# Kernel optimization log

Measured on AMD Instinct MI355X. Metric: run time of the kernel, lower is better.

## Reference

```python
import jax, jax.numpy as jnp
import numpy as np

S = 14          # grid size
B = 2           # boxes per cell
NCLS = 20       # number of classes
L_COORD = 5.0
L_NOOBJ = 0.5


def setup_inputs() -> dict:
    key = jax.random.key(0)
    k1, k2, k3, k4 = jax.random.split(key, 4)
    N = 4096
    pred_tensor = jax.random.uniform(k1, (N, S, S, B * 5 + NCLS), dtype=jnp.float32)
    target_boxes = jax.random.uniform(k2, (N, S, S, 4), dtype=jnp.float32)
    target_cls = jax.random.uniform(k3, (N, S, S, NCLS), dtype=jnp.float32)
    has_object_map = jax.random.randint(k4, (N, S, S), 0, 2) == 1
    return {
        "pred_tensor": pred_tensor,
        "target_boxes": target_boxes,
        "target_cls": target_cls,
        "has_object_map": has_object_map,
    }


def _yolo_loss(pred_tensor, target_boxes, target_cls, has_object_map):
    N = pred_tensor.shape[0]
    inv_n = 1.0 / N
    m = has_object_map.astype(pred_tensor.dtype)            # (N,S,S) 1 where object

    pred_boxes = pred_tensor[..., : B * 5].reshape(*pred_tensor.shape[:3], B, 5)  # (N,S,S,B,5)
    pred_cls = pred_tensor[..., B * 5:]                     # (N,S,S,20)

    # class loss over object cells (masked sum == boolean-index + sum)
    cls_loss = jnp.sum(m[..., None] * (pred_cls - target_cls) ** 2) * inv_n

    # no-object confidence loss: all B confidences at non-object cells vs 0
    conf = pred_boxes[..., 4]                               # (N,S,S,B)
    no_obj_loss = jnp.sum((1.0 - m)[..., None] * conf ** 2) * inv_n

    # per-cell IoU of each of the B predicted boxes against the target box.
    # xywh2xyxy: center x,y are divided by S; w,h used directly (as in source).
    xy = pred_boxes[..., :2] / S                            # (N,S,S,B,2)
    wh = pred_boxes[..., 2:4]                               # (N,S,S,B,2)
    p1 = xy - wh / 2
    p2 = xy + wh / 2
    t = target_boxes[..., None, :]                          # (N,S,S,1,4) treated as xyxy
    lt = jnp.maximum(p1, t[..., :2])
    rb = jnp.minimum(p2, t[..., 2:])
    iwh = jnp.clip(rb - lt, 0.0)
    inter = iwh[..., 0] * iwh[..., 1]                       # (N,S,S,B)
    area_p = wh[..., 0] * wh[..., 1]                        # (x2-x1)*(y2-y1) = w*h
    area_t = (t[..., 2] - t[..., 0]) * (t[..., 3] - t[..., 1])
    iou = inter / (area_p + area_t - inter)                 # (N,S,S,B)

    # best-of-B selection per cell (torch.max picks first max index -> argmax)
    best_idx = jnp.argmax(iou, axis=-1)                     # (N,S,S)
    best_boxes = jnp.take_along_axis(
        pred_boxes, best_idx[..., None, None], axis=3
    )[..., 0, :]                                            # (N,S,S,5)

    # containing-object confidence loss: best conf vs 1.0 at object cells
    containing_obj_loss = jnp.sum(m * (best_boxes[..., 4] - 1.0) ** 2) * inv_n

    center_loss = jnp.sum(m[..., None] * (best_boxes[..., :2] - target_boxes[..., :2]) ** 2)
    dim_loss = jnp.sum(
        m[..., None]
        * (jnp.sqrt(best_boxes[..., 2:4]) - jnp.sqrt(target_boxes[..., 2:4])) ** 2
    )
    reg_loss = (center_loss + dim_loss) * inv_n

    total_loss = cls_loss + L_NOOBJ * no_obj_loss + L_COORD * reg_loss + containing_obj_loss
    # [total, reg, containing_obj, no_obj, cls]
    return jnp.stack([total_loss, reg_loss, containing_obj_loss, no_obj_loss, cls_loss])


def reference(pred_tensor, target_boxes, target_cls, has_object_map):
    return _yolo_loss(pred_tensor, target_boxes, target_cls, has_object_map)
```

## Files before the change

kernel.cpp:

```cpp
#include <hip/hip_runtime.h>


#define NCELLS (4096 * 14 * 14)
#define NBLOCKS (NCELLS / 256)
#define NLINES 32


__global__ void yolo_zero_kernel(float* __restrict__ ws) {
    const int t = threadIdx.x;
#pragma unroll
    for (int i = 0; i < 3; ++i) {
        const int k = t + 256 * i;
        if (k < 544) ws[k] = 0.0f;
    }
}

__global__ void yolo_detect_kernel(const unsigned char* __restrict__ mb,
                                   int* __restrict__ flag) {
    int t = threadIdx.x;
    unsigned int found = 0;
#pragma unroll
    for (int k = 0; k < 16; ++k) {
        int slot = t * 16 + k;
        found |= mb[4 * slot + 1] | mb[4 * slot + 2] | mb[4 * slot + 3];
    }
    if (found) atomicOr(flag, 1);
}

__global__ __launch_bounds__(256) void yolo_main_kernel(
    const float* __restrict__ pred,
    const float* __restrict__ tbox,
    const float* __restrict__ tcls,
    const void* __restrict__ mask,
    const int* __restrict__ flag,
    float* __restrict__ ws) {
    const int c = blockIdx.x * 256 + threadIdx.x;

    float pv[30];
    {
        const float2* p2 = (const float2*)(pred + (long long)30 * c);
#pragma unroll
        for (int k = 0; k < 15; ++k) {
            float2 t = p2[k];
            pv[2 * k] = t.x;
            pv[2 * k + 1] = t.y;
        }
    }
    const float4 tb = *(const float4*)(tbox + (long long)4 * c);
    float tc[20];
    {
        const float4* c4 = (const float4*)(tcls + (long long)20 * c);
#pragma unroll
        for (int k = 0; k < 5; ++k) {
            float4 t = c4[k];
            tc[4 * k] = t.x;
            tc[4 * k + 1] = t.y;
            tc[4 * k + 2] = t.z;
            tc[4 * k + 3] = t.w;
        }
    }
    const int mode = *flag;
    float m;
    if (mode) {
        m = ((const unsigned char*)mask)[c] ? 1.0f : 0.0f;
    } else {
        m = ((const int*)mask)[c] ? 1.0f : 0.0f;
    }

    float s = 0.0f;
#pragma unroll
    for (int i = 0; i < 20; ++i) {
        float d = pv[10 + i] - tc[i];
        s += d * d;
    }
    float cls_s = m * s;

    float conf0 = pv[4], conf1 = pv[9];
    float noobj_s = (1.0f - m) * (conf0 * conf0 + conf1 * conf1);

    float iou[2];
    float at = (tb.z - tb.x) * (tb.w - tb.y);
#pragma unroll
    for (int b = 0; b < 2; ++b) {
        int base = 5 * b;
        float x = pv[base] / 14.0f;
        float y = pv[base + 1] / 14.0f;
        float w = pv[base + 2];
        float h = pv[base + 3];
        float p1x = x - w * 0.5f, p1y = y - h * 0.5f;
        float p2x = x + w * 0.5f, p2y = y + h * 0.5f;
        float ltx = fmaxf(p1x, tb.x), lty = fmaxf(p1y, tb.y);
        float rbx = fminf(p2x, tb.z), rby = fminf(p2y, tb.w);
        float iw = fmaxf(rbx - ltx, 0.0f), ih = fmaxf(rby - lty, 0.0f);
        float inter = iw * ih;
        float ap = w * h;
        iou[b] = inter / (ap + at - inter);
    }
    int best = (iou[1] > iou[0]) ? 5 : 0;
    float bx = pv[best], by = pv[best + 1], bw = pv[best + 2], bh = pv[best + 3],
          bc = pv[best + 4];

    float contain_s = m * (bc - 1.0f) * (bc - 1.0f);

    float dx = bx - tb.x, dy = by - tb.y;
    float dw = sqrtf(bw) - sqrtf(tb.z);
    float dh = sqrtf(bh) - sqrtf(tb.w);
    float reg_s = m * (dx * dx + dy * dy + dw * dw + dh * dh);

#pragma unroll
    for (int off = 32; off > 0; off >>= 1) {
        cls_s += __shfl_down(cls_s, off, 64);
        noobj_s += __shfl_down(noobj_s, off, 64);
        contain_s += __shfl_down(contain_s, off, 64);
        reg_s += __shfl_down(reg_s, off, 64);
    }
    __shared__ float red[4][4];
    int lane = threadIdx.x & 63;
    int wid = threadIdx.x >> 6;
    if (lane == 0) {
        red[wid][0] = cls_s;
        red[wid][1] = noobj_s;
        red[wid][2] = contain_s;
        red[wid][3] = reg_s;
    }
    __syncthreads();
    if (threadIdx.x < 4) {
        float v = red[0][threadIdx.x] + red[1][threadIdx.x] +
                  red[2][threadIdx.x] + red[3][threadIdx.x];
        atomicAdd(&ws[16 * (blockIdx.x & (NLINES - 1)) + threadIdx.x], v);
    }
}

__global__ void yolo_final_kernel(const float* __restrict__ ws,
                                  float* __restrict__ out) {
    const int t = threadIdx.x;
    float4 v = make_float4(0.f, 0.f, 0.f, 0.f);
    if (t < NLINES) v = ((const float4*)ws)[4 * t];
#pragma unroll
    for (int off = 32; off > 0; off >>= 1) {
        v.x += __shfl_down(v.x, off, 64);
        v.y += __shfl_down(v.y, off, 64);
        v.z += __shfl_down(v.z, off, 64);
        v.w += __shfl_down(v.w, off, 64);
    }
    if (t == 0) {
        const float inv_n = 1.0f / 4096.0f;
        const float cls = v.x * inv_n;
        const float noobj = v.y * inv_n;
        const float contain = v.z * inv_n;
        const float reg = v.w * inv_n;
        out[0] = cls + 0.5f * noobj + 5.0f * reg + contain;
        out[1] = reg;
        out[2] = contain;
        out[3] = noobj;
        out[4] = cls;
    }
}

extern "C" void kernel_launch(void* const* d_in, const int* in_sizes, int n_in,
                              void* d_out, int out_size, void* d_ws,
                              size_t ws_size, hipStream_t stream) {
    const float* pred = (const float*)d_in[0];
    const float* tbox = (const float*)d_in[1];
    const float* tcls = (const float*)d_in[2];
    const void* mask = d_in[3];
    float* ws = (float*)d_ws;
    float* out = (float*)d_out;

    yolo_zero_kernel<<<1, 256, 0, stream>>>(ws);
    yolo_detect_kernel<<<1, 256, 0, stream>>>((const unsigned char*)mask,
                                              (int*)(ws + 512));
    yolo_main_kernel<<<NBLOCKS, 256, 0, stream>>>(pred, tbox, tcls, mask,
                                                  (const int*)(ws + 512), ws);
    yolo_final_kernel<<<1, 64, 0, stream>>>(ws, out);
}
```

Measured before the change: 207.5 us.

## Stage prediction rows into LDS via global_load_lds and use per-wave atomics

Result: no change. 208.2 us (+0.4%).

```diff
diff --git a/kernel.cpp b/kernel.cpp
--- a/kernel.cpp
+++ b/kernel.cpp
@@ -3,15 +3,22 @@
 
 #define NCELLS (4096 * 14 * 14)
 #define NBLOCKS (NCELLS / 256)
-#define NLINES 32
+#define NLINES 64
 
+
+typedef const __attribute__((address_space(1))) void* gas_t;
+typedef __attribute__((address_space(3))) void* las_t;
+
+__device__ __forceinline__ void gload_lds16(const void* g, void* l) {
+    __builtin_amdgcn_global_load_lds((gas_t)g, (las_t)l, 16, 0, 0);
+}
 
 __global__ void yolo_zero_kernel(float* __restrict__ ws) {
     const int t = threadIdx.x;
 #pragma unroll
-    for (int i = 0; i < 3; ++i) {
+    for (int i = 0; i < 5; ++i) {
         const int k = t + 256 * i;
-        if (k < 544) ws[k] = 0.0f;
+        if (k < 1040) ws[k] = 0.0f;
     }
 }
 
@@ -34,31 +41,39 @@
     const void* __restrict__ mask,
     const int* __restrict__ flag,
     float* __restrict__ ws) {
-    const int c = blockIdx.x * 256 + threadIdx.x;
+    __shared__ float sp[256 * 30 + 128];
 
-    float pv[30];
+    const int t = threadIdx.x;
+    const int lane = t & 63;
+    const int wid = t >> 6;
+    const int c = blockIdx.x * 256 + t;
+
     {
-        const float2* p2 = (const float2*)(pred + (long long)30 * c);
+        const char* gbase =
+            (const char*)pred + (long long)(blockIdx.x * 256 + wid * 64) * 120;
+        const char* gend = (const char*)pred + (long long)NCELLS * 120;
+        char* lbase = (char*)sp + wid * 7680;
 #pragma unroll
-        for (int k = 0; k < 15; ++k) {
-            float2 t = p2[k];
-            pv[2 * k] = t.x;
-            pv[2 * k + 1] = t.y;
+        for (int k = 0; k < 8; ++k) {
+            const char* src = gbase + k * 1024 + lane * 16;
+            if (src + 16 > gend) src = gend - 16;
+            gload_lds16(src, lbase + k * 1024);
         }
     }
-    const float4 tb = *(const float4*)(tbox + (long long)4 * c);
+
     float tc[20];
     {
         const float4* c4 = (const float4*)(tcls + (long long)20 * c);
 #pragma unroll
         for (int k = 0; k < 5; ++k) {
-            float4 t = c4[k];
-            tc[4 * k] = t.x;
-            tc[4 * k + 1] = t.y;
-            tc[4 * k + 2] = t.z;
-            tc[4 * k + 3] = t.w;
+            float4 v = c4[k];
+            tc[4 * k] = v.x;
+            tc[4 * k + 1] = v.y;
+            tc[4 * k + 2] = v.z;
+            tc[4 * k + 3] = v.w;
         }
     }
+    const float4 tb = *(const float4*)(tbox + (long long)4 * c);
     const int mode = *flag;
     float m;
     if (mode) {
@@ -67,13 +82,22 @@
         m = ((const int*)mask)[c] ? 1.0f : 0.0f;
     }
 
+    asm volatile("s_waitcnt vmcnt(0)" ::: "memory");
+    __builtin_amdgcn_sched_barrier(0);
+
+    const float* pc = sp + wid * 1920 + 30 * lane;
+
     float s = 0.0f;
 #pragma unroll
     for (int i = 0; i < 20; ++i) {
-        float d = pv[10 + i] - tc[i];
+        float d = pc[10 + i] - tc[i];
         s += d * d;
     }
     float cls_s = m * s;
+
+    float pv[10];
+#pragma unroll
+    for (int i = 0; i < 10; ++i) pv[i] = pc[i];
 
     float conf0 = pv[4], conf1 = pv[9];
     float noobj_s = (1.0f - m) * (conf0 * conf0 + conf1 * conf1);
@@ -114,28 +138,19 @@
         contain_s += __shfl_down(contain_s, off, 64);
         reg_s += __shfl_down(reg_s, off, 64);
     }
-    __shared__ float red[4][4];
-    int lane = threadIdx.x & 63;
-    int wid = threadIdx.x >> 6;
     if (lane == 0) {
-        red[wid][0] = cls_s;
-        red[wid][1] = noobj_s;
-        red[wid][2] = contain_s;
-        red[wid][3] = reg_s;
-    }
-    __syncthreads();
-    if (threadIdx.x < 4) {
-        float v = red[0][threadIdx.x] + red[1][threadIdx.x] +
-                  red[2][threadIdx.x] + red[3][threadIdx.x];
-        atomicAdd(&ws[16 * (blockIdx.x & (NLINES - 1)) + threadIdx.x], v);
+        const int line = 16 * (((blockIdx.x << 2) | wid) & (NLINES - 1));
+        atomicAdd(&ws[line + 0], cls_s);
+        atomicAdd(&ws[line + 1], noobj_s);
+        atomicAdd(&ws[line + 2], contain_s);
+        atomicAdd(&ws[line + 3], reg_s);
     }
 }
 
 __global__ void yolo_final_kernel(const float* __restrict__ ws,
                                   float* __restrict__ out) {
     const int t = threadIdx.x;
-    float4 v = make_float4(0.f, 0.f, 0.f, 0.f);
-    if (t < NLINES) v = ((const float4*)ws)[4 * t];
+    float4 v = ((const float4*)ws)[4 * t];
 #pragma unroll
     for (int off = 32; off > 0; off >>= 1) {
         v.x += __shfl_down(v.x, off, 64);
@@ -169,8 +184,8 @@
 
     yolo_zero_kernel<<<1, 256, 0, stream>>>(ws);
     yolo_detect_kernel<<<1, 256, 0, stream>>>((const unsigned char*)mask,
-                                              (int*)(ws + 512));
+                                              (int*)(ws + 1024));
     yolo_main_kernel<<<NBLOCKS, 256, 0, stream>>>(pred, tbox, tcls, mask,
-                                                  (const int*)(ws + 512), ws);
+                                                  (const int*)(ws + 1024), ws);
     yolo_final_kernel<<<1, 64, 0, stream>>>(ws, out);
 }
```
